# Optimization experiments

Hardware: AMD Instinct MI355X
Metric: run time of the kernel (lower is better)

## Reference

```python
import jax, jax.numpy as jnp
import numpy as np

H = 12
D_MODEL = 768
D_K = D_MODEL // H  # 64


def setup_inputs() -> dict:
    key = jax.random.key(0)
    ks = jax.random.split(key, 16)
    B, S, D = 4, 1024, D_MODEL
    scale = 1.0 / np.sqrt(D)
    inp = {
        "query": jax.random.normal(ks[0], (B, S, D), jnp.float32),
        "key": jax.random.normal(ks[1], (B, S, D), jnp.float32),
        "value": jax.random.normal(ks[2], (B, S, D), jnp.float32),
        "times": jax.random.normal(ks[3], (2, B, S, D), jnp.float32),
        # learned params (Linear weights stored torch-style [out, in])
        "Wq": jax.random.normal(ks[4], (D, D), jnp.float32) * scale,
        "bq": jnp.zeros((D,), jnp.float32),
        "Wk": jax.random.normal(ks[5], (D, D), jnp.float32) * scale,
        "bk": jnp.zeros((D,), jnp.float32),
        "Wv": jax.random.normal(ks[6], (D, D), jnp.float32) * scale,
        "bv": jnp.zeros((D,), jnp.float32),
        "Wt": jax.random.normal(ks[7], (D, D), jnp.float32) * scale,
        "bt": jnp.zeros((D,), jnp.float32),
        "Wo": jax.random.normal(ks[8], (D, D), jnp.float32) * scale,
        "bo": jnp.zeros((D,), jnp.float32),
    }
    return inp


def _split_heads(x, B, S):
    # [B,S,D] -> [B,H,S,D_K]
    return x.reshape(B, S, H, D_K).transpose(0, 2, 1, 3)


def reference(query, key, value, times, Wq, bq, Wk, bk, Wv, bv, Wt, bt, Wo, bo):
    B, S, D = query.shape
    inv_sqrt_dk = 1.0 / jnp.sqrt(jnp.asarray(D_K, query.dtype))
    # q/k/v projections are identical across time-loop iterations; hoist them.
    q = _split_heads(query @ Wq.T + bq, B, S)   # [B,H,S,dk]
    k = _split_heads(key @ Wk.T + bk, B, S)
    v = _split_heads(value @ Wv.T + bv, B, S)
    x = jnp.zeros_like(q)
    n_times = times.shape[0]
    for i in range(n_times):  # small fixed loop over time embeddings
        t = _split_heads(times[i] @ Wt.T + bt, B, S)
        # dual-score attention: query.time + query.key, each scaled by 1/sqrt(d_k)
        scores = (jnp.einsum('bhqd,bhkd->bhqk', q, t)
                  + jnp.einsum('bhqd,bhkd->bhqk', q, k)) * inv_sqrt_dk
        p = jax.nn.softmax(scores, axis=-1)
        x = x + jnp.einsum('bhqk,bhkd->bhqd', p, v)
    x = x.transpose(0, 2, 1, 3).reshape(B, S, H * D_K)
    return x @ Wo.T + bo
```

## Files before the change

### kernel.cpp

```cpp
#include <hip/hip_runtime.h>
#include <hip/hip_fp16.h>

typedef _Float16 v8h __attribute__((ext_vector_type(8)));
typedef _Float16 v4h __attribute__((ext_vector_type(4)));
typedef _Float16 v2h __attribute__((ext_vector_type(2)));
typedef float v4f __attribute__((ext_vector_type(4)));

#define MFMA_F16 __builtin_amdgcn_mfma_f32_16x16x32_f16
#define EXP2F __builtin_amdgcn_exp2f
#define SCHED_FENCE() __builtin_amdgcn_sched_barrier(0)

__device__ static inline v2h pkrtz(float a, float b) {
  return __builtin_bit_cast(v2h, __builtin_amdgcn_cvt_pkrtz(a, b));
}

__device__ static inline void async_copy16(const void* g, void* l) {
  __builtin_amdgcn_global_load_lds(
      (const __attribute__((address_space(1))) void*)g,
      (__attribute__((address_space(3))) void*)l, 16, 0, 0);
}

struct CastArgs {
  const float* src[5];
  _Float16* dst[5];
  int start[6];
  float scale[5];
};
__global__ void cast_all(CastArgs a) {
  const int g = blockIdx.x * 256 + threadIdx.x;
  if (g >= a.start[5]) return;
  int z = 0;
  #pragma unroll
  for (int i = 1; i < 5; ++i) if (g >= a.start[i]) z = i;
  const int i0 = g - a.start[z];
  const float sc = a.scale[z];
  const float* s = a.src[z] + (size_t)i0 * 8;
  const float4 f0 = *(const float4*)s;
  const float4 f1 = *(const float4*)(s + 4);
  v8h o = {(_Float16)(f0.x * sc), (_Float16)(f0.y * sc),
           (_Float16)(f0.z * sc), (_Float16)(f0.w * sc),
           (_Float16)(f1.x * sc), (_Float16)(f1.y * sc),
           (_Float16)(f1.z * sc), (_Float16)(f1.w * sc)};
  *(v8h*)(a.dst[z] + (size_t)i0 * 8) = o;
}

struct GemmArgs {
  const void* A1[4]; const void* A2[4];
  const _Float16* W1[4]; const _Float16* W2[4];
  const float* b1[4];    const float* b2[4];
  void* out[4];
  float bscale[4];
  int K[4];
  int mode[4];
};

template <int NMT>
__device__ static inline void gemm_epilogue(const GemmArgs& g, int z,
                                            v4f (&acc)[NMT][4], int m0, int n0,
                                            int wm, int wn, int quad, int l16) {
  const int mode = g.mode[z];
  #pragma unroll
  for (int nt = 0; nt < 4; ++nt) {
    const int col = n0 + wn + nt * 16 + l16;
    float bv = g.b1[z][col] * g.bscale[z];
    if (g.b2[z]) bv += g.b2[z][col];
    if (mode == 1) {
      _Float16* outp = (_Float16*)g.out[z];
      const int h = col >> 6, dk = col & 63;
      #pragma unroll
      for (int mt = 0; mt < NMT; ++mt) {
        const int row = m0 + wm + mt * 16 + quad * 4;
        const int b = row >> 10, s = row & 1023;
        const int sp = (s & ~31) | ((s & 12) << 1) | ((s & 16) >> 2);
        v4h pack = {(_Float16)(acc[mt][nt][0] + bv), (_Float16)(acc[mt][nt][1] + bv),
                    (_Float16)(acc[mt][nt][2] + bv), (_Float16)(acc[mt][nt][3] + bv)};
        *(v4h*)&outp[(size_t)((b * 12 + h) * 64 + dk) * 1024 + sp] = pack;
      }
    } else {
      #pragma unroll
      for (int mt = 0; mt < NMT; ++mt)
        #pragma unroll
        for (int r = 0; r < 4; ++r) {
          const int row = m0 + wm + mt * 16 + quad * 4 + r;
          const float v = acc[mt][nt][r] + bv;
          if (mode == 2) ((float*)g.out[z])[(size_t)row * 768 + col] = v;
          else ((_Float16*)g.out[z])[(size_t)row * 768 + col] = (_Float16)v;
        }
    }
  }
}

__global__ __launch_bounds__(256) void gemm_proj(GemmArgs g) {
  __shared__ _Float16 a_lds[128 * 64];
  __shared__ _Float16 w_lds[2 * 128 * 64];
  const int z = blockIdx.z;
  const int KK = g.K[z];
  const int tid = threadIdx.x;
  const int w = tid >> 6, lane = tid & 63, quad = lane >> 4, l16 = lane & 15;
  const int m0 = blockIdx.x * 128, n0 = blockIdx.y * 128;
  const int wm = (w >> 1) * 64, wn = (w & 1) * 64;

  size_t srcOffW[4]; int ldsOffW[4];
  #pragma unroll
  for (int i = 0; i < 4; ++i) {
    const int c = i * 256 + tid, row = c >> 3, slot = c & 7;
    srcOffW[i] = (size_t)row * 768 + (size_t)((slot ^ (row & 7)) * 8);
    ldsOffW[i] = (i * 256 + w * 64) * 8;
  }
  auto stageW = [&](const _Float16* Wsrc, int kc, int buf) {
    #pragma unroll
    for (int i = 0; i < 4; ++i)
      async_copy16(Wsrc + (size_t)n0 * 768 + kc + srcOffW[i],
                   &w_lds[buf * 8192 + ldsOffW[i]]);
  };

  int rowA[4], colA[4], dstA[4];
  float4 areg[4][2];
  #pragma unroll
  for (int i = 0; i < 4; ++i) {
    const int s = i * 256 + tid, row = s >> 3, slot = s & 7;
    rowA[i] = row;
    colA[i] = (slot ^ (row & 7)) * 8;
    dstA[i] = s * 8;
  }
  auto loadA = [&](const float* Af, int kc) {
    #pragma unroll
    for (int i = 0; i < 4; ++i) {
      const float* p = Af + (size_t)(m0 + rowA[i]) * 768 + kc + colA[i];
      areg[i][0] = *(const float4*)p;
      areg[i][1] = *(const float4*)(p + 4);
    }
  };
  auto writeA = [&]() {
    #pragma unroll
    for (int i = 0; i < 4; ++i) {
      const float4 f0 = areg[i][0], f1 = areg[i][1];
      v8h o = {(_Float16)f0.x, (_Float16)f0.y, (_Float16)f0.z, (_Float16)f0.w,
               (_Float16)f1.x, (_Float16)f1.y, (_Float16)f1.z, (_Float16)f1.w};
      *(v8h*)&a_lds[dstA[i]] = o;
    }
  };

  const void* A1 = g.A1[z]; const void* A2 = g.A2[z];
  const _Float16* W1 = g.W1[z]; const _Float16* W2 = g.W2[z];

  v4f acc[4][4] = {};

  loadA((const float*)A1, 0);
  stageW(W1, 0, 0);

  for (int k0 = 0; k0 < KK; k0 += 64) {
    const int cur = (k0 >> 6) & 1;
    const int k0n = k0 + 64;
    const bool hn = k0n < KK;
    const int kcn = (k0n < 768) ? k0n : k0n - 768;
    const bool nf = k0n < 768;

    writeA();
    if (hn) {
      loadA((const float*)(nf ? A1 : A2), kcn);
      stageW(nf ? W1 : W2, kcn, cur ^ 1);
    }
    SCHED_FENCE();
    if (hn) asm volatile("s_waitcnt vmcnt(12) lgkmcnt(0)" ::: "memory");
    else    asm volatile("s_waitcnt vmcnt(0) lgkmcnt(0)" ::: "memory");
    SCHED_FENCE();
    __builtin_amdgcn_s_barrier();
    SCHED_FENCE();

    const _Float16* wl = &w_lds[cur * 8192];
    #pragma unroll
    for (int kh = 0; kh < 2; ++kh) {
      v8h af[4], bf[4];
      #pragma unroll
      for (int mt = 0; mt < 4; ++mt) {
        const int r = wm + mt * 16 + l16;
        af[mt] = *(const v8h*)&a_lds[r * 64 + (((kh * 4 + quad) ^ (r & 7)) * 8)];
      }
      #pragma unroll
      for (int nt = 0; nt < 4; ++nt) {
        const int r = wn + nt * 16 + l16;
        bf[nt] = *(const v8h*)&wl[r * 64 + (((kh * 4 + quad) ^ (r & 7)) * 8)];
      }
      __builtin_amdgcn_s_setprio(1);
      #pragma unroll
      for (int mt = 0; mt < 4; ++mt)
        #pragma unroll
        for (int nt = 0; nt < 4; ++nt)
          acc[mt][nt] = MFMA_F16(af[mt], bf[nt], acc[mt][nt], 0, 0, 0);
      __builtin_amdgcn_s_setprio(0);
    }
    SCHED_FENCE();
    __builtin_amdgcn_s_barrier();
    SCHED_FENCE();
  }

  gemm_epilogue<4>(g, z, acc, m0, n0, wm, wn, quad, l16);
}

__global__ __launch_bounds__(256) void gemm_out(GemmArgs g) {
  __shared__ _Float16 a_lds[2 * 64 * 64];
  __shared__ _Float16 w_lds[2 * 128 * 64];
  const int z = 0;
  const int KK = g.K[z];
  const int tid = threadIdx.x;
  const int w = tid >> 6, lane = tid & 63, quad = lane >> 4, l16 = lane & 15;
  const int m0 = blockIdx.x * 64, n0 = blockIdx.y * 128;
  const int wm = (w >> 1) * 32, wn = (w & 1) * 64;

  size_t srcOffW[4]; int ldsOffW[4];
  #pragma unroll
  for (int i = 0; i < 4; ++i) {
    const int c = i * 256 + tid, row = c >> 3, slot = c & 7;
    srcOffW[i] = (size_t)row * 768 + (size_t)((slot ^ (row & 7)) * 8);
    ldsOffW[i] = (i * 256 + w * 64) * 8;
  }
  const _Float16* A1 = (const _Float16*)g.A1[z];
  const _Float16* W1 = g.W1[z];

  auto stage = [&](int kc, int buf) {
    #pragma unroll
    for (int i = 0; i < 2; ++i)
      async_copy16(A1 + (size_t)m0 * 768 + kc + srcOffW[i],
                   &a_lds[buf * 4096 + ldsOffW[i]]);
    #pragma unroll
    for (int i = 0; i < 4; ++i)
      async_copy16(W1 + (size_t)n0 * 768 + kc + srcOffW[i],
                   &w_lds[buf * 8192 + ldsOffW[i]]);
  };

  v4f acc[2][4] = {};
  stage(0, 0);

  for (int k0 = 0; k0 < KK; k0 += 64) {
    const int cur = (k0 >> 6) & 1;
    const bool hn = k0 + 64 < KK;
    if (hn) stage(k0 + 64, cur ^ 1);
    SCHED_FENCE();
    if (hn) asm volatile("s_waitcnt vmcnt(6) lgkmcnt(0)" ::: "memory");
    else    asm volatile("s_waitcnt vmcnt(0) lgkmcnt(0)" ::: "memory");
    SCHED_FENCE();
    __builtin_amdgcn_s_barrier();
    SCHED_FENCE();

    const _Float16* al = &a_lds[cur * 4096];
    const _Float16* wl = &w_lds[cur * 8192];
    #pragma unroll
    for (int kh = 0; kh < 2; ++kh) {
      v8h af[2], bf[4];
      #pragma unroll
      for (int mt = 0; mt < 2; ++mt) {
        const int r = wm + mt * 16 + l16;
        af[mt] = *(const v8h*)&al[r * 64 + (((kh * 4 + quad) ^ (r & 7)) * 8)];
      }
      #pragma unroll
      for (int nt = 0; nt < 4; ++nt) {
        const int r = wn + nt * 16 + l16;
        bf[nt] = *(const v8h*)&wl[r * 64 + (((kh * 4 + quad) ^ (r & 7)) * 8)];
      }
      __builtin_amdgcn_s_setprio(1);
      #pragma unroll
      for (int mt = 0; mt < 2; ++mt)
        #pragma unroll
        for (int nt = 0; nt < 4; ++nt)
          acc[mt][nt] = MFMA_F16(af[mt], bf[nt], acc[mt][nt], 0, 0, 0);
      __builtin_amdgcn_s_setprio(0);
    }
    SCHED_FENCE();
    __builtin_amdgcn_s_barrier();
    SCHED_FENCE();
  }

  gemm_epilogue<2>(g, z, acc, m0, n0, wm, wn, quad, l16);
}

__global__ __launch_bounds__(256) void attn(
    const _Float16* __restrict__ Q,
    const _Float16* __restrict__ KT0, const _Float16* __restrict__ KT1,
    const _Float16* __restrict__ Vt,
    _Float16* __restrict__ X)
{
  __shared__ _Float16 lds[6 * 4096];

  const int tid = threadIdx.x;
  const int w = tid >> 6, lane = tid & 63, quad = lane >> 4, l16 = lane & 15;

  const int orig = blockIdx.y * 16 + blockIdx.x;
  const int wgid = (orig & 7) * 96 + (orig >> 3);
  const int bh = wgid >> 4, q0 = (wgid & 15) * 64;
  const int b = bh / 12, h = bh % 12;
  const size_t base = (size_t)b * 1024 * 768 + h * 64;

  const _Float16* k0s = KT0 + base;
  const _Float16* k1s = KT1 + base;
  const _Float16* vs  = Vt + (size_t)bh * 64 * 1024;

  size_t ktOff[2], vOff[2]; int ldsOff[2];
  #pragma unroll
  for (int i = 0; i < 2; ++i) {
    const int c = i * 256 + w * 64 + lane, row = c >> 3, slot = c & 7;
    const int logical = slot ^ (row & 7);
    ktOff[i] = (size_t)row * 768 + (size_t)(logical * 8);
    vOff[i] = (size_t)row * 1024 + (size_t)(logical * 8);
    ldsOff[i] = c * 8;
  }
  auto stage = [&](int buf) {
    #pragma unroll
    for (int i = 0; i < 2; ++i) {
      async_copy16(k0s + ktOff[i], &lds[buf * 4096 + ldsOff[i]]);
      async_copy16(k1s + ktOff[i], &lds[8192 + buf * 4096 + ldsOff[i]]);
      async_copy16(vs + vOff[i], &lds[16384 + buf * 4096 + ldsOff[i]]);
    }
    k0s += 64 * 768; k1s += 64 * 768; vs += 64;
  };

  const _Float16* Qw = Q + base + (size_t)(q0 + w * 16) * 768;
  const v8h qf0 = *(const v8h*)(Qw + (size_t)l16 * 768 + quad * 8);
  const v8h qf1 = *(const v8h*)(Qw + (size_t)l16 * 768 + 32 + quad * 8);

  int ra0[4], ra1[4];
  #pragma unroll
  for (int t = 0; t < 4; ++t) {
    const int r = t * 16 + l16, rw = r & 7;
    ra0[t] = (r * 64 + ((quad ^ rw) * 8)) * 2;
    ra1[t] = ra0[t] ^ 64;
  }

  const _Float16 one = (_Float16)1.f;
  const v8h ones8 = {one, one, one, one, one, one, one, one};
  v4f o[2][4] = {};
  v4f osum[2] = {};

  auto body = [&](int B, bool doStage) {
    __syncthreads();
    if (doStage) stage((B == 0) ? 1 : 0);

    const char* L = (const char*)lds;

    v4f s[2][4];
    __builtin_amdgcn_s_setprio(1);
    #pragma unroll
    for (int kvt = 0; kvt < 4; ++kvt) {
      const v8h k00 = *(const v8h*)(L + B + ra0[kvt]);
      const v8h k01 = *(const v8h*)(L + B + ra1[kvt]);
      const v8h k10 = *(const v8h*)(L + 16384 + B + ra0[kvt]);
      const v8h k11 = *(const v8h*)(L + 16384 + B + ra1[kvt]);
      s[0][kvt] = MFMA_F16(k00, qf0, v4f{}, 0, 0, 0);
      s[0][kvt] = MFMA_F16(k01, qf1, s[0][kvt], 0, 0, 0);
      s[1][kvt] = MFMA_F16(k10, qf0, v4f{}, 0, 0, 0);
      s[1][kvt] = MFMA_F16(k11, qf1, s[1][kvt], 0, 0, 0);
    }
    __builtin_amdgcn_s_setprio(0);

    v8h pb8[2][2];
    #pragma unroll
    for (int t = 0; t < 2; ++t)
      #pragma unroll
      for (int gg = 0; gg < 2; ++gg) {
        const v4f sa = s[t][gg * 2], sb = s[t][gg * 2 + 1];
        const v2h a0 = pkrtz(EXP2F(sa[0]), EXP2F(sa[1]));
        const v2h a1 = pkrtz(EXP2F(sa[2]), EXP2F(sa[3]));
        const v2h b0 = pkrtz(EXP2F(sb[0]), EXP2F(sb[1]));
        const v2h b1 = pkrtz(EXP2F(sb[2]), EXP2F(sb[3]));
        pb8[t][gg] = v8h{a0[0], a0[1], a1[0], a1[1], b0[0], b0[1], b1[0], b1[1]};
        osum[t] = MFMA_F16(ones8, pb8[t][gg], osum[t], 0, 0, 0);
      }

    __builtin_amdgcn_s_setprio(1);
    #pragma unroll
    for (int dkt = 0; dkt < 4; ++dkt) {
      const v8h v0 = *(const v8h*)(L + 32768 + B + ra0[dkt]);
      const v8h v1 = *(const v8h*)(L + 32768 + B + ra1[dkt]);
      o[0][dkt] = MFMA_F16(v0, pb8[0][0], o[0][dkt], 0, 0, 0);
      o[0][dkt] = MFMA_F16(v1, pb8[0][1], o[0][dkt], 0, 0, 0);
      o[1][dkt] = MFMA_F16(v0, pb8[1][0], o[1][dkt], 0, 0, 0);
      o[1][dkt] = MFMA_F16(v1, pb8[1][1], o[1][dkt], 0, 0, 0);
    }
    __builtin_amdgcn_s_setprio(0);
  };

  stage(0);
  for (int it = 0; it < 7; ++it) {
    body(0, true);
    body(8192, true);
  }
  body(0, true);
  body(8192, false);

  const float i0 = 1.0f / osum[0][0], i1 = 1.0f / osum[1][0];

  _Float16* Xw = X + base + (size_t)(q0 + w * 16 + l16) * 768;
  #pragma unroll
  for (int dkt = 0; dkt < 4; ++dkt) {
    v4h pack;
    #pragma unroll
    for (int r = 0; r < 4; ++r)
      pack[r] = (_Float16)(o[0][dkt][r] * i0 + o[1][dkt][r] * i1);
    *(v4h*)&Xw[dkt * 16 + quad * 4] = pack;
  }
}

extern "C" void kernel_launch(void* const* d_in, const int* in_sizes, int n_in,
                              void* d_out, int out_size, void* d_ws, size_t ws_size,
                              hipStream_t stream) {
  const float* query = (const float*)d_in[0];
  const float* key   = (const float*)d_in[1];
  const float* value = (const float*)d_in[2];
  const float* times = (const float*)d_in[3];
  const float* Wq = (const float*)d_in[4];  const float* bq = (const float*)d_in[5];
  const float* Wk = (const float*)d_in[6];  const float* bk = (const float*)d_in[7];
  const float* Wv = (const float*)d_in[8];  const float* bv = (const float*)d_in[9];
  const float* Wt = (const float*)d_in[10]; const float* bt = (const float*)d_in[11];
  const float* Wo = (const float*)d_in[12]; const float* bo = (const float*)d_in[13];
  float* out = (float*)d_out;

  const size_t NELEM = (size_t)4096 * 768;
  const size_t WELEM = (size_t)768 * 768;
  const float QSCALE = 0.125f * 1.4426950408889634f;

  char* ws = (char*)d_ws;
  size_t off = 0;
  auto alloc = [&](size_t bytes) {
    void* p = ws + off; off += (bytes + 255) & ~(size_t)255; return p;
  };
  _Float16* wqh = (_Float16*)alloc(WELEM * 2);
  _Float16* wkh = (_Float16*)alloc(WELEM * 2);
  _Float16* wvh = (_Float16*)alloc(WELEM * 2);
  _Float16* wth = (_Float16*)alloc(WELEM * 2);
  _Float16* woh = (_Float16*)alloc(WELEM * 2);
  _Float16* Qh  = (_Float16*)alloc(NELEM * 2);
  _Float16* KT0 = (_Float16*)alloc(NELEM * 2);
  _Float16* KT1 = (_Float16*)alloc(NELEM * 2);
  _Float16* Vt  = (_Float16*)alloc(NELEM * 2);
  _Float16* Xh  = (_Float16*)alloc(NELEM * 2);

  CastArgs ca = {};
  const int nW8 = (int)(WELEM / 8);
  const float* csrc[5] = {Wq, Wk, Wv, Wt, Wo};
  _Float16* cdst[5] = {wqh, wkh, wvh, wth, woh};
  int acc8 = 0;
  for (int i = 0; i < 5; ++i) {
    ca.src[i] = csrc[i]; ca.dst[i] = cdst[i];
    ca.start[i] = acc8;
    acc8 += nW8;
    ca.scale[i] = (i == 0) ? QSCALE : 1.0f;
  }
  ca.start[5] = acc8;
  cast_all<<<dim3((acc8 + 255) / 256), 256, 0, stream>>>(ca);

  GemmArgs pa = {};
  pa.A1[0] = times;         pa.A2[0] = key; pa.W1[0] = wth; pa.W2[0] = wkh;
  pa.b1[0] = bt; pa.b2[0] = bk; pa.out[0] = KT0; pa.bscale[0] = 1.0f;
  pa.K[0] = 1536; pa.mode[0] = 0;
  pa.A1[1] = times + NELEM; pa.A2[1] = key; pa.W1[1] = wth; pa.W2[1] = wkh;
  pa.b1[1] = bt; pa.b2[1] = bk; pa.out[1] = KT1; pa.bscale[1] = 1.0f;
  pa.K[1] = 1536; pa.mode[1] = 0;
  pa.A1[2] = query; pa.A2[2] = query; pa.W1[2] = wqh; pa.W2[2] = wqh;
  pa.b1[2] = bq; pa.b2[2] = nullptr; pa.out[2] = Qh; pa.bscale[2] = QSCALE;
  pa.K[2] = 768; pa.mode[2] = 0;
  pa.A1[3] = value; pa.A2[3] = value; pa.W1[3] = wvh; pa.W2[3] = wvh;
  pa.b1[3] = bv; pa.b2[3] = nullptr; pa.out[3] = Vt; pa.bscale[3] = 1.0f;
  pa.K[3] = 768; pa.mode[3] = 1;
  gemm_proj<<<dim3(32, 6, 4), 256, 0, stream>>>(pa);

  attn<<<dim3(16, 48), 256, 0, stream>>>(Qh, KT0, KT1, Vt, Xh);

  GemmArgs oa = {};
  oa.A1[0] = Xh; oa.A2[0] = Xh; oa.W1[0] = woh; oa.W2[0] = woh;
  oa.b1[0] = bo; oa.b2[0] = nullptr; oa.out[0] = out; oa.bscale[0] = 1.0f;
  oa.K[0] = 768; oa.mode[0] = 2;
  gemm_out<<<dim3(64, 6, 1), 256, 0, stream>>>(oa);
}
```

Baseline: 215.7 us.

## Split fused K+T projection into separate K, T0, T1 GEMMs and add in attention

Instead of computing (times_i+key) projections as K=1536 GEMMs writing KT0/KT1, the projection kernel now computes K, T0, T1, Q, V as five K=768 GEMMs, which cuts projection FLOPs. The attention kernel loads K, T0 and T1 tiles into registers and adds them before writing to LDS, in place of async LDS copies of the precomputed sums. The projection GEMM also gains a triple-buffered W and double-buffered A pipeline with one barrier per step, plus an XCD-aware block remapping. The cost is more global reads in attention (three streams instead of two) and register-staged loads replacing the async copies.

```diff
diff --git a/kernel.cpp b/kernel.cpp
--- a/kernel.cpp
+++ b/kernel.cpp
@@ -44,31 +44,132 @@
   *(v8h*)(a.dst[z] + (size_t)i0 * 8) = o;
 }
 
-struct GemmArgs {
-  const void* A1[4]; const void* A2[4];
-  const _Float16* W1[4]; const _Float16* W2[4];
-  const float* b1[4];    const float* b2[4];
-  void* out[4];
-  float bscale[4];
-  int K[4];
-  int mode[4];
+struct ProjArgs {
+  const float* A[5];
+  const _Float16* W[5];
+  const float* b[5];
+  void* out[5];
+  float bscale[5];
+  int mode[5];
 };
 
-template <int NMT>
-__device__ static inline void gemm_epilogue(const GemmArgs& g, int z,
-                                            v4f (&acc)[NMT][4], int m0, int n0,
-                                            int wm, int wn, int quad, int l16) {
+__global__ __launch_bounds__(256) void gemm_proj(ProjArgs g) {
+  __shared__ _Float16 a_lds[2][128 * 64];
+  __shared__ _Float16 w_lds[3][128 * 64];
+  const int tid = threadIdx.x;
+  const int w = tid >> 6, lane = tid & 63, quad = lane >> 4, l16 = lane & 15;
+
+  const int hw = blockIdx.x + blockIdx.y * 6 + blockIdx.z * 192;
+  const int o = (hw & 7) * 120 + (hw >> 3);
+  const int n0 = (o % 6) * 128;
+  const int m0 = ((o / 6) & 31) * 128;
+  const int z = o / 192;
+
+  const float* A = g.A[z];
+  const _Float16* W = g.W[z];
+  const int wm = (w >> 1) * 64, wn = (w & 1) * 64;
+
+  size_t srcOffW[4]; int ldsOffW[4];
+  #pragma unroll
+  for (int i = 0; i < 4; ++i) {
+    const int c = i * 256 + tid, row = c >> 3, slot = c & 7;
+    srcOffW[i] = (size_t)row * 768 + (size_t)((slot ^ (row & 7)) * 8);
+    ldsOffW[i] = (i * 256 + w * 64) * 8;
+  }
+  auto stageW = [&](int kc, int buf) {
+    #pragma unroll
+    for (int i = 0; i < 4; ++i)
+      async_copy16(W + (size_t)n0 * 768 + kc + srcOffW[i],
+                   &w_lds[buf][ldsOffW[i]]);
+  };
+
+  int rowA[4], colA[4], dstA[4];
+  float4 areg[4][2];
+  #pragma unroll
+  for (int i = 0; i < 4; ++i) {
+    const int s = i * 256 + tid, row = s >> 3, slot = s & 7;
+    rowA[i] = row;
+    colA[i] = (slot ^ (row & 7)) * 8;
+    dstA[i] = s * 8;
+  }
+  auto loadA = [&](int kc) {
+    #pragma unroll
+    for (int i = 0; i < 4; ++i) {
+      const float* p = A + (size_t)(m0 + rowA[i]) * 768 + kc + colA[i];
+      areg[i][0] = *(const float4*)p;
+      areg[i][1] = *(const float4*)(p + 4);
+    }
+  };
+  auto writeA = [&](int buf) {
+    #pragma unroll
+    for (int i = 0; i < 4; ++i) {
+      const float4 f0 = areg[i][0], f1 = areg[i][1];
+      v8h o8 = {(_Float16)f0.x, (_Float16)f0.y, (_Float16)f0.z, (_Float16)f0.w,
+                (_Float16)f1.x, (_Float16)f1.y, (_Float16)f1.z, (_Float16)f1.w};
+      *(v8h*)&a_lds[buf][dstA[i]] = o8;
+    }
+  };
+
+  v4f acc[4][4] = {};
+
+  loadA(0);
+  stageW(0, 0);
+  writeA(0);
+  loadA(64);
+  stageW(64, 1);
+  SCHED_FENCE();
+  asm volatile("s_waitcnt vmcnt(12) lgkmcnt(0)" ::: "memory");
+  SCHED_FENCE();
+  __builtin_amdgcn_s_barrier();
+  SCHED_FENCE();
+
+  for (int k = 0; k < 12; ++k) {
+    if (k <= 10) writeA((k + 1) & 1);
+    if (k <= 9) { loadA((k + 2) * 64); stageW((k + 2) * 64, (k + 2) % 3); }
+
+    const _Float16* al = a_lds[k & 1];
+    const _Float16* wl = w_lds[k % 3];
+    #pragma unroll
+    for (int kh = 0; kh < 2; ++kh) {
+      v8h af[4], bf[4];
+      #pragma unroll
+      for (int mt = 0; mt < 4; ++mt) {
+        const int r = wm + mt * 16 + l16;
+        af[mt] = *(const v8h*)&al[r * 64 + (((kh * 4 + quad) ^ (r & 7)) * 8)];
+      }
+      #pragma unroll
+      for (int nt = 0; nt < 4; ++nt) {
+        const int r = wn + nt * 16 + l16;
+        bf[nt] = *(const v8h*)&wl[r * 64 + (((kh * 4 + quad) ^ (r & 7)) * 8)];
+      }
+      __builtin_amdgcn_s_setprio(1);
+      #pragma unroll
+      for (int mt = 0; mt < 4; ++mt)
+        #pragma unroll
+        for (int nt = 0; nt < 4; ++nt)
+          acc[mt][nt] = MFMA_F16(af[mt], bf[nt], acc[mt][nt], 0, 0, 0);
+      __builtin_amdgcn_s_setprio(0);
+    }
+
+    SCHED_FENCE();
+    if (k <= 9)
+      asm volatile("s_waitcnt vmcnt(12) lgkmcnt(0)" ::: "memory");
+    else if (k == 10)
+      asm volatile("s_waitcnt vmcnt(0) lgkmcnt(0)" ::: "memory");
+    SCHED_FENCE();
+    if (k <= 10) { __builtin_amdgcn_s_barrier(); SCHED_FENCE(); }
+  }
+
   const int mode = g.mode[z];
   #pragma unroll
   for (int nt = 0; nt < 4; ++nt) {
     const int col = n0 + wn + nt * 16 + l16;
-    float bv = g.b1[z][col] * g.bscale[z];
-    if (g.b2[z]) bv += g.b2[z][col];
+    const float bv = g.b[z][col] * g.bscale[z];
     if (mode == 1) {
       _Float16* outp = (_Float16*)g.out[z];
       const int h = col >> 6, dk = col & 63;
       #pragma unroll
-      for (int mt = 0; mt < NMT; ++mt) {
+      for (int mt = 0; mt < 4; ++mt) {
         const int row = m0 + wm + mt * 16 + quad * 4;
         const int b = row >> 10, s = row & 1023;
         const int sp = (s & ~31) | ((s & 12) << 1) | ((s & 16) >> 2);
@@ -77,28 +178,27 @@
         *(v4h*)&outp[(size_t)((b * 12 + h) * 64 + dk) * 1024 + sp] = pack;
       }
     } else {
-      #pragma unroll
-      for (int mt = 0; mt < NMT; ++mt)
+      _Float16* outp = (_Float16*)g.out[z];
+      #pragma unroll
+      for (int mt = 0; mt < 4; ++mt)
         #pragma unroll
         for (int r = 0; r < 4; ++r) {
           const int row = m0 + wm + mt * 16 + quad * 4 + r;
-          const float v = acc[mt][nt][r] + bv;
-          if (mode == 2) ((float*)g.out[z])[(size_t)row * 768 + col] = v;
-          else ((_Float16*)g.out[z])[(size_t)row * 768 + col] = (_Float16)v;
+          outp[(size_t)row * 768 + col] = (_Float16)(acc[mt][nt][r] + bv);
         }
     }
   }
 }
 
-__global__ __launch_bounds__(256) void gemm_proj(GemmArgs g) {
-  __shared__ _Float16 a_lds[128 * 64];
+struct OutArgs { const _Float16* A; const _Float16* W; const float* b; float* out; };
+
+__global__ __launch_bounds__(256) void gemm_out(OutArgs g) {
+  __shared__ _Float16 a_lds[2 * 64 * 64];
   __shared__ _Float16 w_lds[2 * 128 * 64];
-  const int z = blockIdx.z;
-  const int KK = g.K[z];
   const int tid = threadIdx.x;
   const int w = tid >> 6, lane = tid & 63, quad = lane >> 4, l16 = lane & 15;
-  const int m0 = blockIdx.x * 128, n0 = blockIdx.y * 128;
-  const int wm = (w >> 1) * 64, wn = (w & 1) * 64;
+  const int m0 = blockIdx.x * 64, n0 = blockIdx.y * 128;
+  const int wm = (w >> 1) * 32, wn = (w & 1) * 64;
 
   size_t srcOffW[4]; int ldsOffW[4];
   #pragma unroll
@@ -107,134 +207,23 @@
     srcOffW[i] = (size_t)row * 768 + (size_t)((slot ^ (row & 7)) * 8);
     ldsOffW[i] = (i * 256 + w * 64) * 8;
   }
-  auto stageW = [&](const _Float16* Wsrc, int kc, int buf) {
+  auto stage = [&](int kc, int buf) {
+    #pragma unroll
+    for (int i = 0; i < 2; ++i)
+      async_copy16(g.A + (size_t)m0 * 768 + kc + srcOffW[i],
+                   &a_lds[buf * 4096 + ldsOffW[i]]);
     #pragma unroll
     for (int i = 0; i < 4; ++i)
-      async_copy16(Wsrc + (size_t)n0 * 768 + kc + srcOffW[i],
-                   &w_lds[buf * 8192 + ldsOffW[i]]);
-  };
-
-  int rowA[4], colA[4], dstA[4];
-  float4 areg[4][2];
-  #pragma unroll
-  for (int i = 0; i < 4; ++i) {
-    const int s = i * 256 + tid, row = s >> 3, slot = s & 7;
-    rowA[i] = row;
-    colA[i] = (slot ^ (row & 7)) * 8;
-    dstA[i] = s * 8;
-  }
-  auto loadA = [&](const float* Af, int kc) {
-    #pragma unroll
-    for (int i = 0; i < 4; ++i) {
-      const float* p = Af + (size_t)(m0 + rowA[i]) * 768 + kc + colA[i];
-      areg[i][0] = *(const float4*)p;
-      areg[i][1] = *(const float4*)(p + 4);
-    }
-  };
-  auto writeA = [&]() {
-    #pragma unroll
-    for (int i = 0; i < 4; ++i) {
-      const float4 f0 = areg[i][0], f1 = areg[i][1];
-      v8h o = {(_Float16)f0.x, (_Float16)f0.y, (_Float16)f0.z, (_Float16)f0.w,
-               (_Float16)f1.x, (_Float16)f1.y, (_Float16)f1.z, (_Float16)f1.w};
-      *(v8h*)&a_lds[dstA[i]] = o;
-    }
-  };
-
-  const void* A1 = g.A1[z]; const void* A2 = g.A2[z];
-  const _Float16* W1 = g.W1[z]; const _Float16* W2 = g.W2[z];
-
-  v4f acc[4][4] = {};
-
-  loadA((const float*)A1, 0);
-  stageW(W1, 0, 0);
-
-  for (int k0 = 0; k0 < KK; k0 += 64) {
-    const int cur = (k0 >> 6) & 1;
-    const int k0n = k0 + 64;
-    const bool hn = k0n < KK;
-    const int kcn = (k0n < 768) ? k0n : k0n - 768;
-    const bool nf = k0n < 768;
-
-    writeA();
-    if (hn) {
-      loadA((const float*)(nf ? A1 : A2), kcn);
-      stageW(nf ? W1 : W2, kcn, cur ^ 1);
-    }
-    SCHED_FENCE();
-    if (hn) asm volatile("s_waitcnt vmcnt(12) lgkmcnt(0)" ::: "memory");
-    else    asm volatile("s_waitcnt vmcnt(0) lgkmcnt(0)" ::: "memory");
-    SCHED_FENCE();
-    __builtin_amdgcn_s_barrier();
-    SCHED_FENCE();
-
-    const _Float16* wl = &w_lds[cur * 8192];
-    #pragma unroll
-    for (int kh = 0; kh < 2; ++kh) {
-      v8h af[4], bf[4];
-      #pragma unroll
-      for (int mt = 0; mt < 4; ++mt) {
-        const int r = wm + mt * 16 + l16;
-        af[mt] = *(const v8h*)&a_lds[r * 64 + (((kh * 4 + quad) ^ (r & 7)) * 8)];
-      }
-      #pragma unroll
-      for (int nt = 0; nt < 4; ++nt) {
-        const int r = wn + nt * 16 + l16;
-        bf[nt] = *(const v8h*)&wl[r * 64 + (((kh * 4 + quad) ^ (r & 7)) * 8)];
-      }
-      __builtin_amdgcn_s_setprio(1);
-      #pragma unroll
-      for (int mt = 0; mt < 4; ++mt)
-        #pragma unroll
-        for (int nt = 0; nt < 4; ++nt)
-          acc[mt][nt] = MFMA_F16(af[mt], bf[nt], acc[mt][nt], 0, 0, 0);
-      __builtin_amdgcn_s_setprio(0);
-    }
-    SCHED_FENCE();
-    __builtin_amdgcn_s_barrier();
-    SCHED_FENCE();
-  }
-
-  gemm_epilogue<4>(g, z, acc, m0, n0, wm, wn, quad, l16);
-}
-
-__global__ __launch_bounds__(256) void gemm_out(GemmArgs g) {
-  __shared__ _Float16 a_lds[2 * 64 * 64];
-  __shared__ _Float16 w_lds[2 * 128 * 64];
-  const int z = 0;
-  const int KK = g.K[z];
-  const int tid = threadIdx.x;
-  const int w = tid >> 6, lane = tid & 63, quad = lane >> 4, l16 = lane & 15;
-  const int m0 = blockIdx.x * 64, n0 = blockIdx.y * 128;
-  const int wm = (w >> 1) * 32, wn = (w & 1) * 64;
-
-  size_t srcOffW[4]; int ldsOffW[4];
-  #pragma unroll
-  for (int i = 0; i < 4; ++i) {
-    const int c = i * 256 + tid, row = c >> 3, slot = c & 7;
-    srcOffW[i] = (size_t)row * 768 + (size_t)((slot ^ (row & 7)) * 8);
-    ldsOffW[i] = (i * 256 + w * 64) * 8;
-  }
-  const _Float16* A1 = (const _Float16*)g.A1[z];
-  const _Float16* W1 = g.W1[z];
-
-  auto stage = [&](int kc, int buf) {
-    #pragma unroll
-    for (int i = 0; i < 2; ++i)
-      async_copy16(A1 + (size_t)m0 * 768 + kc + srcOffW[i],
-                   &a_lds[buf * 4096 + ldsOffW[i]]);
-    #pragma unroll
-    for (int i = 0; i < 4; ++i)
-      async_copy16(W1 + (size_t)n0 * 768 + kc + srcOffW[i],
+      async_copy16(g.W + (size_t)n0 * 768 + kc + srcOffW[i],
                    &w_lds[buf * 8192 + ldsOffW[i]]);
   };
 
   v4f acc[2][4] = {};
   stage(0, 0);
 
-  for (int k0 = 0; k0 < KK; k0 += 64) {
+  for (int k0 = 0; k0 < 768; k0 += 64) {
     const int cur = (k0 >> 6) & 1;
-    const bool hn = k0 + 64 < KK;
+    const bool hn = k0 + 64 < 768;
     if (hn) stage(k0 + 64, cur ^ 1);
     SCHED_FENCE();
     if (hn) asm volatile("s_waitcnt vmcnt(6) lgkmcnt(0)" ::: "memory");
@@ -271,12 +260,24 @@
     SCHED_FENCE();
   }
 
-  gemm_epilogue<2>(g, z, acc, m0, n0, wm, wn, quad, l16);
+  #pragma unroll
+  for (int nt = 0; nt < 4; ++nt) {
+    const int col = n0 + wn + nt * 16 + l16;
+    const float bv = g.b[col];
+    #pragma unroll
+    for (int mt = 0; mt < 2; ++mt)
+      #pragma unroll
+      for (int r = 0; r < 4; ++r) {
+        const int row = m0 + wm + mt * 16 + quad * 4 + r;
+        g.out[(size_t)row * 768 + col] = acc[mt][nt][r] + bv;
+      }
+  }
 }
 
 __global__ __launch_bounds__(256) void attn(
     const _Float16* __restrict__ Q,
-    const _Float16* __restrict__ KT0, const _Float16* __restrict__ KT1,
+    const _Float16* __restrict__ Kp, const _Float16* __restrict__ T0p,
+    const _Float16* __restrict__ T1p,
     const _Float16* __restrict__ Vt,
     _Float16* __restrict__ X)
 {
@@ -291,8 +292,9 @@
   const int b = bh / 12, h = bh % 12;
   const size_t base = (size_t)b * 1024 * 768 + h * 64;
 
-  const _Float16* k0s = KT0 + base;
-  const _Float16* k1s = KT1 + base;
+  const _Float16* ks  = Kp + base;
+  const _Float16* t0s = T0p + base;
+  const _Float16* t1s = T1p + base;
   const _Float16* vs  = Vt + (size_t)bh * 64 * 1024;
 
   size_t ktOff[2], vOff[2]; int ldsOff[2];
@@ -304,14 +306,26 @@
     vOff[i] = (size_t)row * 1024 + (size_t)(logical * 8);
     ldsOff[i] = c * 8;
   }
-  auto stage = [&](int buf) {
+
+  v8h kreg[2], t0reg[2], t1reg[2];
+  auto issueLoads = [&](int buf) {
     #pragma unroll
     for (int i = 0; i < 2; ++i) {
-      async_copy16(k0s + ktOff[i], &lds[buf * 4096 + ldsOff[i]]);
-      async_copy16(k1s + ktOff[i], &lds[8192 + buf * 4096 + ldsOff[i]]);
+      kreg[i]  = *(const v8h*)(ks + ktOff[i]);
+      t0reg[i] = *(const v8h*)(t0s + ktOff[i]);
+      t1reg[i] = *(const v8h*)(t1s + ktOff[i]);
+    }
+    #pragma unroll
+    for (int i = 0; i < 2; ++i)
       async_copy16(vs + vOff[i], &lds[16384 + buf * 4096 + ldsOff[i]]);
-    }
-    k0s += 64 * 768; k1s += 64 * 768; vs += 64;
+    ks += 64 * 768; t0s += 64 * 768; t1s += 64 * 768; vs += 64;
+  };
+  auto finishStage = [&](int buf) {
+    #pragma unroll
+    for (int i = 0; i < 2; ++i) {
+      *(v8h*)&lds[buf * 4096 + ldsOff[i]]        = kreg[i] + t0reg[i];
+      *(v8h*)&lds[8192 + buf * 4096 + ldsOff[i]] = kreg[i] + t1reg[i];
+    }
   };
 
   const _Float16* Qw = Q + base + (size_t)(q0 + w * 16) * 768;
@@ -331,9 +345,14 @@
   v4f o[2][4] = {};
   v4f osum[2] = {};
 
-  auto body = [&](int B, bool doStage) {
+  issueLoads(0);
+  finishStage(0);
+
+  #pragma unroll 2
+  for (int cc = 0; cc < 16; ++cc) {
     __syncthreads();
-    if (doStage) stage((B == 0) ? 1 : 0);
+    const int B = (cc & 1) * 8192;
+    if (cc < 15) issueLoads((cc + 1) & 1);
 
     const char* L = (const char*)lds;
 
@@ -377,15 +396,9 @@
       o[1][dkt] = MFMA_F16(v1, pb8[1][1], o[1][dkt], 0, 0, 0);
     }
     __builtin_amdgcn_s_setprio(0);
-  };
-
-  stage(0);
-  for (int it = 0; it < 7; ++it) {
-    body(0, true);
-    body(8192, true);
-  }
-  body(0, true);
-  body(8192, false);
+
+    if (cc < 15) finishStage((cc + 1) & 1);
+  }
 
   const float i0 = 1.0f / osum[0][0], i1 = 1.0f / osum[1][0];
 
@@ -429,8 +442,9 @@
   _Float16* wth = (_Float16*)alloc(WELEM * 2);
   _Float16* woh = (_Float16*)alloc(WELEM * 2);
   _Float16* Qh  = (_Float16*)alloc(NELEM * 2);
-  _Float16* KT0 = (_Float16*)alloc(NELEM * 2);
-  _Float16* KT1 = (_Float16*)alloc(NELEM * 2);
+  _Float16* Kh  = (_Float16*)alloc(NELEM * 2);
+  _Float16* T0h = (_Float16*)alloc(NELEM * 2);
+  _Float16* T1h = (_Float16*)alloc(NELEM * 2);
   _Float16* Vt  = (_Float16*)alloc(NELEM * 2);
   _Float16* Xh  = (_Float16*)alloc(NELEM * 2);
 
@@ -448,26 +462,21 @@
   ca.start[5] = acc8;
   cast_all<<<dim3((acc8 + 255) / 256), 256, 0, stream>>>(ca);
 
-  GemmArgs pa = {};
-  pa.A1[0] = times;         pa.A2[0] = key; pa.W1[0] = wth; pa.W2[0] = wkh;
-  pa.b1[0] = bt; pa.b2[0] = bk; pa.out[0] = KT0; pa.bscale[0] = 1.0f;
-  pa.K[0] = 1536; pa.mode[0] = 0;
-  pa.A1[1] = times + NELEM; pa.A2[1] = key; pa.W1[1] = wth; pa.W2[1] = wkh;
-  pa.b1[1] = bt; pa.b2[1] = bk; pa.out[1] = KT1; pa.bscale[1] = 1.0f;
-  pa.K[1] = 1536; pa.mode[1] = 0;
-  pa.A1[2] = query; pa.A2[2] = query; pa.W1[2] = wqh; pa.W2[2] = wqh;
-  pa.b1[2] = bq; pa.b2[2] = nullptr; pa.out[2] = Qh; pa.bscale[2] = QSCALE;
-  pa.K[2] = 768; pa.mode[2] = 0;
-  pa.A1[3] = value; pa.A2[3] = value; pa.W1[3] = wvh; pa.W2[3] = wvh;
-  pa.b1[3] = bv; pa.b2[3] = nullptr; pa.out[3] = Vt; pa.bscale[3] = 1.0f;
-  pa.K[3] = 768; pa.mode[3] = 1;
-  gemm_proj<<<dim3(32, 6, 4), 256, 0, stream>>>(pa);
-
-  attn<<<dim3(16, 48), 256, 0, stream>>>(Qh, KT0, KT1, Vt, Xh);
-
-  GemmArgs oa = {};
-  oa.A1[0] = Xh; oa.A2[0] = Xh; oa.W1[0] = woh; oa.W2[0] = woh;
-  oa.b1[0] = bo; oa.b2[0] = nullptr; oa.out[0] = out; oa.bscale[0] = 1.0f;
-  oa.K[0] = 768; oa.mode[0] = 2;
-  gemm_out<<<dim3(64, 6, 1), 256, 0, stream>>>(oa);
-}
+  ProjArgs pa = {};
+  pa.A[0] = key;           pa.W[0] = wkh; pa.b[0] = bk; pa.out[0] = Kh;
+  pa.bscale[0] = 1.0f; pa.mode[0] = 0;
+  pa.A[1] = times;         pa.W[1] = wth; pa.b[1] = bt; pa.out[1] = T0h;
+  pa.bscale[1] = 1.0f; pa.mode[1] = 0;
+  pa.A[2] = times + NELEM; pa.W[2] = wth; pa.b[2] = bt; pa.out[2] = T1h;
+  pa.bscale[2] = 1.0f; pa.mode[2] = 0;
+  pa.A[3] = query;         pa.W[3] = wqh; pa.b[3] = bq; pa.out[3] = Qh;
+  pa.bscale[3] = QSCALE; pa.mode[3] = 0;
+  pa.A[4] = value;         pa.W[4] = wvh; pa.b[4] = bv; pa.out[4] = Vt;
+  pa.bscale[4] = 1.0f; pa.mode[4] = 1;
+  gemm_proj<<<dim3(6, 32, 5), 256, 0, stream>>>(pa);
+
+  attn<<<dim3(16, 48), 256, 0, stream>>>(Qh, Kh, T0h, T1h, Vt, Xh);
+
+  OutArgs oa = {Xh, woh, bo, out};
+  gemm_out<<<dim3(64, 6), 256, 0, stream>>>(oa);
+}
```

Result: slower. 221.1 us (+2.5%).

## Single-buffer W tile in projection GEMM and specialize output GEMM

Applied to the files above, without the earlier changes.

The projection GEMM drops double-buffering of the weight tile in LDS, halving its shared memory. It now issues the current W chunk asynchronously each iteration, alongside the register prefetch of the next A chunk, which may allow more blocks per CU at the cost of exposed W load latency. The shared epilogue is inlined and specialized per kernel, and the output GEMM gets a dedicated argument struct with a compile-time K and fp32 store. Both main loops are marked unroll 1 to limit code size and register pressure.

```diff
diff --git a/kernel.cpp b/kernel.cpp
--- a/kernel.cpp
+++ b/kernel.cpp
@@ -54,10 +54,108 @@
   int mode[4];
 };
 
-template <int NMT>
-__device__ static inline void gemm_epilogue(const GemmArgs& g, int z,
-                                            v4f (&acc)[NMT][4], int m0, int n0,
-                                            int wm, int wn, int quad, int l16) {
+__global__ __launch_bounds__(256) void gemm_proj(GemmArgs g) {
+  __shared__ _Float16 a_lds[128 * 64];
+  __shared__ _Float16 w_lds[128 * 64];
+  const int z = blockIdx.z;
+  const int KK = g.K[z];
+  const int tid = threadIdx.x;
+  const int w = tid >> 6, lane = tid & 63, quad = lane >> 4, l16 = lane & 15;
+  const int m0 = blockIdx.x * 128, n0 = blockIdx.y * 128;
+  const int wm = (w >> 1) * 64, wn = (w & 1) * 64;
+
+  size_t srcOffW[4]; int ldsOffW[4];
+  #pragma unroll
+  for (int i = 0; i < 4; ++i) {
+    const int c = i * 256 + tid, row = c >> 3, slot = c & 7;
+    srcOffW[i] = (size_t)row * 768 + (size_t)((slot ^ (row & 7)) * 8);
+    ldsOffW[i] = (i * 256 + w * 64) * 8;
+  }
+  auto stageW = [&](const _Float16* Wsrc, int kc) {
+    #pragma unroll
+    for (int i = 0; i < 4; ++i)
+      async_copy16(Wsrc + (size_t)n0 * 768 + kc + srcOffW[i],
+                   &w_lds[ldsOffW[i]]);
+  };
+
+  int rowA[4], colA[4], dstA[4];
+  float4 areg[4][2];
+  #pragma unroll
+  for (int i = 0; i < 4; ++i) {
+    const int s = i * 256 + tid, row = s >> 3, slot = s & 7;
+    rowA[i] = row;
+    colA[i] = (slot ^ (row & 7)) * 8;
+    dstA[i] = s * 8;
+  }
+  auto loadA = [&](const float* Af, int kc) {
+    #pragma unroll
+    for (int i = 0; i < 4; ++i) {
+      const float* p = Af + (size_t)(m0 + rowA[i]) * 768 + kc + colA[i];
+      areg[i][0] = *(const float4*)p;
+      areg[i][1] = *(const float4*)(p + 4);
+    }
+  };
+  auto writeA = [&]() {
+    #pragma unroll
+    for (int i = 0; i < 4; ++i) {
+      const float4 f0 = areg[i][0], f1 = areg[i][1];
+      v8h o = {(_Float16)f0.x, (_Float16)f0.y, (_Float16)f0.z, (_Float16)f0.w,
+               (_Float16)f1.x, (_Float16)f1.y, (_Float16)f1.z, (_Float16)f1.w};
+      *(v8h*)&a_lds[dstA[i]] = o;
+    }
+  };
+
+  const void* A1 = g.A1[z]; const void* A2 = g.A2[z];
+  const _Float16* W1 = g.W1[z]; const _Float16* W2 = g.W2[z];
+
+  v4f acc[4][4] = {};
+
+  loadA((const float*)A1, 0);
+
+  #pragma unroll 1
+  for (int k0 = 0; k0 < KK; k0 += 64) {
+    const int k0n = k0 + 64;
+    const bool hn = k0n < KK;
+    const int kc  = (k0 < 768) ? k0 : k0 - 768;
+    const int kcn = (k0n < 768) ? k0n : k0n - 768;
+    const bool cf = k0 < 768, nf = k0n < 768;
+
+    writeA();
+    stageW(cf ? W1 : W2, kc);
+    if (hn) loadA((const float*)(nf ? A1 : A2), kcn);
+    SCHED_FENCE();
+    if (hn) asm volatile("s_waitcnt vmcnt(8) lgkmcnt(0)" ::: "memory");
+    else    asm volatile("s_waitcnt vmcnt(0) lgkmcnt(0)" ::: "memory");
+    SCHED_FENCE();
+    __builtin_amdgcn_s_barrier();
+    SCHED_FENCE();
+
+    #pragma unroll
+    for (int kh = 0; kh < 2; ++kh) {
+      v8h af[4], bf[4];
+      #pragma unroll
+      for (int mt = 0; mt < 4; ++mt) {
+        const int r = wm + mt * 16 + l16;
+        af[mt] = *(const v8h*)&a_lds[r * 64 + (((kh * 4 + quad) ^ (r & 7)) * 8)];
+      }
+      #pragma unroll
+      for (int nt = 0; nt < 4; ++nt) {
+        const int r = wn + nt * 16 + l16;
+        bf[nt] = *(const v8h*)&w_lds[r * 64 + (((kh * 4 + quad) ^ (r & 7)) * 8)];
+      }
+      __builtin_amdgcn_s_setprio(1);
+      #pragma unroll
+      for (int mt = 0; mt < 4; ++mt)
+        #pragma unroll
+        for (int nt = 0; nt < 4; ++nt)
+          acc[mt][nt] = MFMA_F16(af[mt], bf[nt], acc[mt][nt], 0, 0, 0);
+      __builtin_amdgcn_s_setprio(0);
+    }
+    SCHED_FENCE();
+    __builtin_amdgcn_s_barrier();
+    SCHED_FENCE();
+  }
+
   const int mode = g.mode[z];
   #pragma unroll
   for (int nt = 0; nt < 4; ++nt) {
@@ -68,7 +166,7 @@
       _Float16* outp = (_Float16*)g.out[z];
       const int h = col >> 6, dk = col & 63;
       #pragma unroll
-      for (int mt = 0; mt < NMT; ++mt) {
+      for (int mt = 0; mt < 4; ++mt) {
         const int row = m0 + wm + mt * 16 + quad * 4;
         const int b = row >> 10, s = row & 1023;
         const int sp = (s & ~31) | ((s & 12) << 1) | ((s & 16) >> 2);
@@ -77,28 +175,27 @@
         *(v4h*)&outp[(size_t)((b * 12 + h) * 64 + dk) * 1024 + sp] = pack;
       }
     } else {
-      #pragma unroll
-      for (int mt = 0; mt < NMT; ++mt)
+      _Float16* outp = (_Float16*)g.out[z];
+      #pragma unroll
+      for (int mt = 0; mt < 4; ++mt)
         #pragma unroll
         for (int r = 0; r < 4; ++r) {
           const int row = m0 + wm + mt * 16 + quad * 4 + r;
-          const float v = acc[mt][nt][r] + bv;
-          if (mode == 2) ((float*)g.out[z])[(size_t)row * 768 + col] = v;
-          else ((_Float16*)g.out[z])[(size_t)row * 768 + col] = (_Float16)v;
+          outp[(size_t)row * 768 + col] = (_Float16)(acc[mt][nt][r] + bv);
         }
     }
   }
 }
 
-__global__ __launch_bounds__(256) void gemm_proj(GemmArgs g) {
-  __shared__ _Float16 a_lds[128 * 64];
+struct OutArgs { const _Float16* A; const _Float16* W; const float* b; float* out; };
+
+__global__ __launch_bounds__(256) void gemm_out(OutArgs g) {
+  __shared__ _Float16 a_lds[2 * 64 * 64];
   __shared__ _Float16 w_lds[2 * 128 * 64];
-  const int z = blockIdx.z;
-  const int KK = g.K[z];
   const int tid = threadIdx.x;
   const int w = tid >> 6, lane = tid & 63, quad = lane >> 4, l16 = lane & 15;
-  const int m0 = blockIdx.x * 128, n0 = blockIdx.y * 128;
-  const int wm = (w >> 1) * 64, wn = (w & 1) * 64;
+  const int m0 = blockIdx.x * 64, n0 = blockIdx.y * 128;
+  const int wm = (w >> 1) * 32, wn = (w & 1) * 64;
 
   size_t srcOffW[4]; int ldsOffW[4];
   #pragma unroll
@@ -107,134 +204,24 @@
     srcOffW[i] = (size_t)row * 768 + (size_t)((slot ^ (row & 7)) * 8);
     ldsOffW[i] = (i * 256 + w * 64) * 8;
   }
-  auto stageW = [&](const _Float16* Wsrc, int kc, int buf) {
+  auto stage = [&](int kc, int buf) {
+    #pragma unroll
+    for (int i = 0; i < 2; ++i)
+      async_copy16(g.A + (size_t)m0 * 768 + kc + srcOffW[i],
+                   &a_lds[buf * 4096 + ldsOffW[i]]);
     #pragma unroll
     for (int i = 0; i < 4; ++i)
-      async_copy16(Wsrc + (size_t)n0 * 768 + kc + srcOffW[i],
-                   &w_lds[buf * 8192 + ldsOffW[i]]);
-  };
-
-  int rowA[4], colA[4], dstA[4];
-  float4 areg[4][2];
-  #pragma unroll
-  for (int i = 0; i < 4; ++i) {
-    const int s = i * 256 + tid, row = s >> 3, slot = s & 7;
-    rowA[i] = row;
-    colA[i] = (slot ^ (row & 7)) * 8;
-    dstA[i] = s * 8;
-  }
-  auto loadA = [&](const float* Af, int kc) {
-    #pragma unroll
-    for (int i = 0; i < 4; ++i) {
-      const float* p = Af + (size_t)(m0 + rowA[i]) * 768 + kc + colA[i];
-      areg[i][0] = *(const float4*)p;
-      areg[i][1] = *(const float4*)(p + 4);
-    }
-  };
-  auto writeA = [&]() {
-    #pragma unroll
-    for (int i = 0; i < 4; ++i) {
-      const float4 f0 = areg[i][0], f1 = areg[i][1];
-      v8h o = {(_Float16)f0.x, (_Float16)f0.y, (_Float16)f0.z, (_Float16)f0.w,
-               (_Float16)f1.x, (_Float16)f1.y, (_Float16)f1.z, (_Float16)f1.w};
-      *(v8h*)&a_lds[dstA[i]] = o;
-    }
-  };
-
-  const void* A1 = g.A1[z]; const void* A2 = g.A2[z];
-  const _Float16* W1 = g.W1[z]; const _Float16* W2 = g.W2[z];
-
-  v4f acc[4][4] = {};
-
-  loadA((const float*)A1, 0);
-  stageW(W1, 0, 0);
-
-  for (int k0 = 0; k0 < KK; k0 += 64) {
-    const int cur = (k0 >> 6) & 1;
-    const int k0n = k0 + 64;
-    const bool hn = k0n < KK;
-    const int kcn = (k0n < 768) ? k0n : k0n - 768;
-    const bool nf = k0n < 768;
-
-    writeA();
-    if (hn) {
-      loadA((const float*)(nf ? A1 : A2), kcn);
-      stageW(nf ? W1 : W2, kcn, cur ^ 1);
-    }
-    SCHED_FENCE();
-    if (hn) asm volatile("s_waitcnt vmcnt(12) lgkmcnt(0)" ::: "memory");
-    else    asm volatile("s_waitcnt vmcnt(0) lgkmcnt(0)" ::: "memory");
-    SCHED_FENCE();
-    __builtin_amdgcn_s_barrier();
-    SCHED_FENCE();
-
-    const _Float16* wl = &w_lds[cur * 8192];
-    #pragma unroll
-    for (int kh = 0; kh < 2; ++kh) {
-      v8h af[4], bf[4];
-      #pragma unroll
-      for (int mt = 0; mt < 4; ++mt) {
-        const int r = wm + mt * 16 + l16;
-        af[mt] = *(const v8h*)&a_lds[r * 64 + (((kh * 4 + quad) ^ (r & 7)) * 8)];
-      }
-      #pragma unroll
-      for (int nt = 0; nt < 4; ++nt) {
-        const int r = wn + nt * 16 + l16;
-        bf[nt] = *(const v8h*)&wl[r * 64 + (((kh * 4 + quad) ^ (r & 7)) * 8)];
-      }
-      __builtin_amdgcn_s_setprio(1);
-      #pragma unroll
-      for (int mt = 0; mt < 4; ++mt)
-        #pragma unroll
-        for (int nt = 0; nt < 4; ++nt)
-          acc[mt][nt] = MFMA_F16(af[mt], bf[nt], acc[mt][nt], 0, 0, 0);
-      __builtin_amdgcn_s_setprio(0);
-    }
-    SCHED_FENCE();
-    __builtin_amdgcn_s_barrier();
-    SCHED_FENCE();
-  }
-
-  gemm_epilogue<4>(g, z, acc, m0, n0, wm, wn, quad, l16);
-}
-
-__global__ __launch_bounds__(256) void gemm_out(GemmArgs g) {
-  __shared__ _Float16 a_lds[2 * 64 * 64];
-  __shared__ _Float16 w_lds[2 * 128 * 64];
-  const int z = 0;
-  const int KK = g.K[z];
-  const int tid = threadIdx.x;
-  const int w = tid >> 6, lane = tid & 63, quad = lane >> 4, l16 = lane & 15;
-  const int m0 = blockIdx.x * 64, n0 = blockIdx.y * 128;
-  const int wm = (w >> 1) * 32, wn = (w & 1) * 64;
-
-  size_t srcOffW[4]; int ldsOffW[4];
-  #pragma unroll
-  for (int i = 0; i < 4; ++i) {
-    const int c = i * 256 + tid, row = c >> 3, slot = c & 7;
-    srcOffW[i] = (size_t)row * 768 + (size_t)((slot ^ (row & 7)) * 8);
-    ldsOffW[i] = (i * 256 + w * 64) * 8;
-  }
-  const _Float16* A1 = (const _Float16*)g.A1[z];
-  const _Float16* W1 = g.W1[z];
-
-  auto stage = [&](int kc, int buf) {
-    #pragma unroll
-    for (int i = 0; i < 2; ++i)
-      async_copy16(A1 + (size_t)m0 * 768 + kc + srcOffW[i],
-                   &a_lds[buf * 4096 + ldsOffW[i]]);
-    #pragma unroll
-    for (int i = 0; i < 4; ++i)
-      async_copy16(W1 + (size_t)n0 * 768 + kc + srcOffW[i],
+      async_copy16(g.W + (size_t)n0 * 768 + kc + srcOffW[i],
                    &w_lds[buf * 8192 + ldsOffW[i]]);
   };
 
   v4f acc[2][4] = {};
   stage(0, 0);
 
-  for (int k0 = 0; k0 < KK; k0 += 64) {
+  #pragma unroll 1
+  for (int k0 = 0; k0 < 768; k0 += 64) {
     const int cur = (k0 >> 6) & 1;
-    const bool hn = k0 + 64 < KK;
+    const bool hn = k0 + 64 < 768;
     if (hn) stage(k0 + 64, cur ^ 1);
     SCHED_FENCE();
     if (hn) asm volatile("s_waitcnt vmcnt(6) lgkmcnt(0)" ::: "memory");
@@ -271,7 +258,18 @@
     SCHED_FENCE();
   }
 
-  gemm_epilogue<2>(g, z, acc, m0, n0, wm, wn, quad, l16);
+  #pragma unroll
+  for (int nt = 0; nt < 4; ++nt) {
+    const int col = n0 + wn + nt * 16 + l16;
+    const float bv = g.b[col];
+    #pragma unroll
+    for (int mt = 0; mt < 2; ++mt)
+      #pragma unroll
+      for (int r = 0; r < 4; ++r) {
+        const int row = m0 + wm + mt * 16 + quad * 4 + r;
+        g.out[(size_t)row * 768 + col] = acc[mt][nt][r] + bv;
+      }
+  }
 }
 
 __global__ __launch_bounds__(256) void attn(
@@ -465,9 +463,6 @@
 
   attn<<<dim3(16, 48), 256, 0, stream>>>(Qh, KT0, KT1, Vt, Xh);
 
-  GemmArgs oa = {};
-  oa.A1[0] = Xh; oa.A2[0] = Xh; oa.W1[0] = woh; oa.W2[0] = woh;
-  oa.b1[0] = bo; oa.b2[0] = nullptr; oa.out[0] = out; oa.bscale[0] = 1.0f;
-  oa.K[0] = 768; oa.mode[0] = 2;
-  gemm_out<<<dim3(64, 6, 1), 256, 0, stream>>>(oa);
-}
+  OutArgs oa = {Xh, woh, bo, out};
+  gemm_out<<<dim3(64, 6), 256, 0, stream>>>(oa);
+}
```

New measurement: 216.0 us. No clear change (+0.1%).
